# Performance work log

Hardware: AMD Instinct MI355X
Metric: run time of the kernel (lower is better)

## Reference

```python
import jax, jax.numpy as jnp
import numpy as np

H = 128          # hidden_channels
N_USER = 100000
N_ITEM = 50000
E = 1000000      # number of labeled edges


def setup_inputs() -> dict:
    key = jax.random.key(0)
    ks = jax.random.split(key, 6)
    z_user = jax.random.normal(ks[0], (N_USER, H), dtype=jnp.float32)
    z_item = jax.random.normal(ks[1], (N_ITEM, H), dtype=jnp.float32)
    row = jax.random.randint(ks[2], (E,), 0, N_USER, dtype=jnp.int64 if jax.config.jax_enable_x64 else jnp.int32)
    col = jax.random.randint(ks[3], (E,), 0, N_ITEM, dtype=jnp.int64 if jax.config.jax_enable_x64 else jnp.int32)
    W1 = jax.random.normal(ks[4], (2 * H, H), dtype=jnp.float32) / np.sqrt(2 * H)
    b1 = jnp.zeros((H,), dtype=jnp.float32)
    W2 = jax.random.normal(ks[5], (H, 1), dtype=jnp.float32) / np.sqrt(H)
    b2 = jnp.zeros((1,), dtype=jnp.float32)
    return {"z_user": z_user, "z_item": z_item, "row": row, "col": col,
            "W1": W1, "b1": b1, "W2": W2, "b2": b2}


def reference(z_user, z_item, row, col, W1, b1, W2, b2):
    # z = cat([z_user[row], z_item[col]], -1); lin1(z).relu(); lin2 -> view(-1)
    # Split W1 so we never materialize the [E, 2H] concat explicitly as one buffer:
    # cat([a, b]) @ W1 == a @ W1[:H] + b @ W1[H:]
    W1u, W1i = W1[:H], W1[H:]
    h = z_user[row] @ W1u + z_item[col] @ W1i + b1          # [E, H]
    h = jax.nn.relu(h)
    out = h @ W2 + b2                                        # [E, 1]
    return out.reshape(-1)
```

## Files before the change

kernel.cpp:

```cpp
#include <hip/hip_runtime.h>

#define HH 128
#define BU 8
#define BI 16
#define NBKT (BU * BI)
#define SCHUNK 2048
#define GPUC 8192

typedef __attribute__((ext_vector_type(8))) short bf16x8;
typedef __attribute__((ext_vector_type(4))) float f32x4;
typedef _Float16 h2 __attribute__((ext_vector_type(2)));

#if __has_builtin(__builtin_amdgcn_fdot2)
#define FDOT2(a, b, c) __builtin_amdgcn_fdot2((a), (b), (c), false)
#else
#define FDOT2(a, b, c) ((c) + (float)(a)[0] * (float)(b)[0] + (float)(a)[1] * (float)(b)[1])
#endif

__device__ inline unsigned short f2bf(float f) {
    unsigned u = __builtin_bit_cast(unsigned, f);
    u += 0x7FFF + ((u >> 16) & 1);
    return (unsigned short)(u >> 16);
}
__device__ inline unsigned short f2h(float f) {
    return __builtin_bit_cast(unsigned short, (_Float16)f);
}

__global__ __launch_bounds__(256) void wt_kernel(
    const float* __restrict__ W1, unsigned short* __restrict__ Wt)
{
    const int gid = blockIdx.x * 256 + threadIdx.x;
    const int h   = gid >> 11;
    const int c   = (gid >> 4) & 127;
    const int kc  = gid & 15;
    const float* src = W1 + (size_t)(h * 128 + kc * 8) * HH + c;
    unsigned short v[8];
    #pragma unroll
    for (int d = 0; d < 8; ++d)
        v[d] = f2bf(src[(size_t)d * HH]);
    uint4 pack;
    pack.x = (unsigned)v[0] | ((unsigned)v[1] << 16);
    pack.y = (unsigned)v[2] | ((unsigned)v[3] << 16);
    pack.z = (unsigned)v[4] | ((unsigned)v[5] << 16);
    pack.w = (unsigned)v[6] | ((unsigned)v[7] << 16);
    *(uint4*)(Wt + (size_t)h * 16384 + c * 128 + ((kc ^ (c & 15)) << 3)) = pack;
}

__global__ __launch_bounds__(256) void scatter_kernel(
    const int* __restrict__ row, const int* __restrict__ col,
    unsigned* __restrict__ cursor, unsigned* __restrict__ srt,
    unsigned* __restrict__ invpos, int E, unsigned n_user, unsigned n_item, int cap)
{
    __shared__ unsigned lh[NBKT];
    __shared__ unsigned gb[NBKT];
    __shared__ unsigned lc[NBKT];
    const int t    = threadIdx.x;
    const int base = blockIdx.x * SCHUNK;

    int uu[SCHUNK / 256], ii[SCHUNK / 256];
    if (t < NBKT) lh[t] = 0;
    __syncthreads();
    #pragma unroll
    for (int k = 0; k < SCHUNK / 256; ++k) {
        int e = base + k * 256 + t;
        if (e < E) {
            uu[k] = row[e]; ii[k] = col[e];
            unsigned uc = ((unsigned)uu[k] * BU) / n_user;
            unsigned ic = ((unsigned)ii[k] * BI) / n_item;
            atomicAdd(&lh[uc * BI + ic], 1u);
        }
    }
    __syncthreads();
    if (t < NBKT) {
        gb[t] = lh[t] ? (unsigned)(t * cap) + atomicAdd(&cursor[t], lh[t]) : 0u;
        lc[t] = 0;
    }
    __syncthreads();
    #pragma unroll
    for (int k = 0; k < SCHUNK / 256; ++k) {
        int e = base + k * 256 + t;
        if (e < E) {
            unsigned uc = ((unsigned)uu[k] * BU) / n_user;
            unsigned ic = ((unsigned)ii[k] * BI) / n_item;
            int b = (int)(uc * BI + ic);
            unsigned ucbase = (uc * n_user + 7u) >> 3;
            unsigned r   = atomicAdd(&lc[b], 1u);
            unsigned pos = gb[b] + r;
            srt[pos]  = (((unsigned)uu[k] - ucbase) << 16) | (unsigned)ii[k];
            invpos[e] = pos;
        }
    }
}

__global__ __launch_bounds__(256) void project_kernel(
    const float* __restrict__ Zu, const float* __restrict__ Zi,
    const unsigned short* __restrict__ Wt, const float* __restrict__ b1,
    unsigned short* __restrict__ Pu, unsigned short* __restrict__ Pi,
    int n_user, int n_item, int utiles, int itiles)
{
    __shared__ unsigned short sWt[128 * 128];
    __shared__ unsigned short sOut[64 * 136];

    const int t    = threadIdx.x;
    const int wave = t >> 6;
    const int lane = t & 63;
    const int l16  = lane & 15;
    const int lk8  = (lane >> 4) * 8;
    const int total = utiles + itiles;

    int staged = -1;

    for (int tid = blockIdx.x; tid < total; tid += gridDim.x) {
        const bool isUser = (tid < utiles);
        const int  half   = isUser ? 0 : 1;
        const float* __restrict__ Z = isUser ? Zu : Zi;
        unsigned short* __restrict__ P = isUser ? Pu : Pi;
        const int nrows = isUser ? n_user : n_item;
        const int rbase = (isUser ? tid : (tid - utiles)) << 6;

        if (half != staged) {
            __syncthreads();
            const unsigned short* src = Wt + (size_t)half * 16384;
            #pragma unroll
            for (int i = 0; i < 16; ++i) {
                int off = (i * 256 + t) * 8;
                *(uint4*)(sWt + off) = *(const uint4*)(src + off);
            }
            __syncthreads();
            staged = half;
        }

        float b1r[8];
        #pragma unroll
        for (int nt = 0; nt < 8; ++nt)
            b1r[nt] = isUser ? b1[nt * 16 + l16] : 0.f;

        f32x4 acc[8];
        #pragma unroll
        for (int nt = 0; nt < 8; ++nt) acc[nt] = (f32x4)0.f;

        int m = rbase + wave * 16 + l16;
        if (m > nrows - 1) m = nrows - 1;
        const float* Zrow = Z + (size_t)m * HH;

        #pragma unroll
        for (int kk = 0; kk < 4; ++kk) {
            float4 z0 = *(const float4*)(Zrow + kk * 32 + lk8);
            float4 z1 = *(const float4*)(Zrow + kk * 32 + lk8 + 4);
            bf16x8 a;
            a[0] = (short)f2bf(z0.x); a[1] = (short)f2bf(z0.y);
            a[2] = (short)f2bf(z0.z); a[3] = (short)f2bf(z0.w);
            a[4] = (short)f2bf(z1.x); a[5] = (short)f2bf(z1.y);
            a[6] = (short)f2bf(z1.z); a[7] = (short)f2bf(z1.w);

            const int chunkSw = ((kk * 4 + (lane >> 4)) ^ l16) << 3;
            #pragma unroll
            for (int nt = 0; nt < 8; ++nt) {
                int c = nt * 16 + l16;
                bf16x8 b = *(const bf16x8*)(sWt + c * 128 + chunkSw);
                acc[nt] = __builtin_amdgcn_mfma_f32_16x16x32_bf16(a, b, acc[nt], 0, 0, 0);
            }
        }

        __syncthreads();
        #pragma unroll
        for (int nt = 0; nt < 8; ++nt) {
            int colc = nt * 16 + l16;
            #pragma unroll
            for (int r = 0; r < 4; ++r) {
                int orow = wave * 16 + (lane >> 4) * 4 + r;
                sOut[orow * 136 + colc] = f2h(acc[nt][r] + b1r[nt]);
            }
        }
        __syncthreads();
        #pragma unroll
        for (int i = 0; i < 4; ++i) {
            int idx = t + i * 256;
            int r   = idx >> 4;
            int ch  = idx & 15;
            int grow = rbase + r;
            if (grow < nrows)
                *(uint4*)(P + (size_t)grow * HH + ch * 8) =
                    *(const uint4*)(sOut + r * 136 + ch * 8);
        }
    }
}

__global__ __launch_bounds__(256) void edge_sorted_kernel(
    const unsigned short* __restrict__ Pu, const unsigned short* __restrict__ Pi,
    const unsigned* __restrict__ srt, const unsigned* __restrict__ cursor,
    const float* __restrict__ W2, const float* __restrict__ b2,
    float* __restrict__ psorted, int cap, int n_user)
{
    const int uc     = blockIdx.x & (BU - 1);
    const int jj     = blockIdx.x >> 3;
    const int g      = threadIdx.x >> 3;
    const int lane8  = threadIdx.x & 7;
    const int gg     = jj * 32 + g;
    const int c0     = lane8 * 16;
    const int ucbase = (int)(((unsigned)uc * (unsigned)n_user + 7u) >> 3);

    h2 w2h[8];
    #pragma unroll
    for (int j = 0; j < 8; ++j) {
        w2h[j][0] = (_Float16)W2[c0 + 2 * j];
        w2h[j][1] = (_Float16)W2[c0 + 2 * j + 1];
    }
    const float b2s = b2[0];
    const h2 hz = {(_Float16)0, (_Float16)0};

    #pragma unroll 1
    for (int ic = 0; ic < BI; ++ic) {
        const int b    = uc * BI + ic;
        const int S    = b * cap;
        const int Tend = S + (int)cursor[b];
        for (int p = S + gg; p < Tend; p += GPUC) {
            unsigned pk = srt[p];
            int u  = ucbase + (int)(pk >> 16);
            int it = (int)(pk & 0xFFFFu);
            const unsigned short* pur = Pu + (size_t)u  * HH + c0;
            const unsigned short* pir = Pi + (size_t)it * HH + c0;
            uint4 a0 = *(const uint4*)pur;
            uint4 a1 = *(const uint4*)(pur + 8);
            uint4 c0v = *(const uint4*)pir;
            uint4 c1v = *(const uint4*)(pir + 8);
            unsigned aw[8] = {a0.x, a0.y, a0.z, a0.w, a1.x, a1.y, a1.z, a1.w};
            unsigned cw[8] = {c0v.x, c0v.y, c0v.z, c0v.w, c1v.x, c1v.y, c1v.z, c1v.w};
            float acc = 0.f;
            #pragma unroll
            for (int q = 0; q < 8; ++q) {
                h2 s = __builtin_bit_cast(h2, aw[q]) + __builtin_bit_cast(h2, cw[q]);
                s = __builtin_elementwise_max(s, hz);
                acc = FDOT2(s, w2h[q], acc);
            }
            acc += __shfl_xor(acc, 4, 64);
            acc += __shfl_xor(acc, 2, 64);
            acc += __shfl_xor(acc, 1, 64);
            if (lane8 == 0) psorted[p] = acc + b2s;
        }
    }
}

__global__ __launch_bounds__(256) void permute_kernel(
    const float* __restrict__ psorted, const unsigned* __restrict__ invpos,
    float* __restrict__ out, int E)
{
    int i  = blockIdx.x * blockDim.x + threadIdx.x;
    int st = gridDim.x * blockDim.x;
    for (int e = i; e < E; e += st)
        out[e] = psorted[invpos[e]];
}

__global__ __launch_bounds__(256) void edge_fp16_kernel(
    const unsigned short* __restrict__ Pu, const unsigned short* __restrict__ Pi,
    const int* __restrict__ row, const int* __restrict__ col,
    const float* __restrict__ W2, const float* __restrict__ b2,
    float* __restrict__ out, int E)
{
    const int lane8  = threadIdx.x & 7;
    const int gid    = (blockIdx.x * blockDim.x + threadIdx.x) >> 3;
    const int stride = (gridDim.x * blockDim.x) >> 3;
    const int c0     = lane8 * 16;

    h2 w2h[8];
    #pragma unroll
    for (int j = 0; j < 8; ++j) {
        w2h[j][0] = (_Float16)W2[c0 + 2 * j];
        w2h[j][1] = (_Float16)W2[c0 + 2 * j + 1];
    }
    const float b2s = b2[0];
    const h2 hz = {(_Float16)0, (_Float16)0};

    for (int e = gid; e < E; e += stride) {
        int u = row[e], it = col[e];
        const unsigned short* pur = Pu + (size_t)u  * HH + c0;
        const unsigned short* pir = Pi + (size_t)it * HH + c0;
        uint4 a0 = *(const uint4*)pur;
        uint4 a1 = *(const uint4*)(pur + 8);
        uint4 c0v = *(const uint4*)pir;
        uint4 c1v = *(const uint4*)(pir + 8);
        unsigned aw[8] = {a0.x, a0.y, a0.z, a0.w, a1.x, a1.y, a1.z, a1.w};
        unsigned cw[8] = {c0v.x, c0v.y, c0v.z, c0v.w, c1v.x, c1v.y, c1v.z, c1v.w};
        float acc = 0.f;
        #pragma unroll
        for (int q = 0; q < 8; ++q) {
            h2 s = __builtin_bit_cast(h2, aw[q]) + __builtin_bit_cast(h2, cw[q]);
            s = __builtin_elementwise_max(s, hz);
            acc = FDOT2(s, w2h[q], acc);
        }
        acc += __shfl_xor(acc, 4, 64);
        acc += __shfl_xor(acc, 2, 64);
        acc += __shfl_xor(acc, 1, 64);
        if (lane8 == 0) out[e] = acc + b2s;
    }
}

__global__ __launch_bounds__(256) void edge_direct_kernel(
    const float* __restrict__ zu, const float* __restrict__ zi,
    const int* __restrict__ row, const int* __restrict__ col,
    const float* __restrict__ W1, const float* __restrict__ b1,
    const float* __restrict__ W2, const float* __restrict__ b2,
    float* __restrict__ out, int E)
{
    const int lane   = threadIdx.x & 31;
    const int gid    = (blockIdx.x * blockDim.x + threadIdx.x) >> 5;
    const int stride = (gridDim.x * blockDim.x) >> 5;
    const int c0     = lane * 4;

    const float4 b1v = *(const float4*)(b1 + c0);
    const float4 w2v = *(const float4*)(W2 + c0);
    const float  b2s = b2[0];

    for (int e = gid; e < E; e += stride) {
        int u  = row[e];
        int it = col[e];
        const float* zur = zu + (size_t)u  * HH;
        const float* zir = zi + (size_t)it * HH;
        float4 acc = b1v;
        for (int k = 0; k < HH; ++k) {
            float  zk = zur[k];
            float4 w  = *(const float4*)(W1 + (size_t)k * HH + c0);
            acc.x = fmaf(zk, w.x, acc.x);
            acc.y = fmaf(zk, w.y, acc.y);
            acc.z = fmaf(zk, w.z, acc.z);
            acc.w = fmaf(zk, w.w, acc.w);
        }
        for (int k = 0; k < HH; ++k) {
            float  zk = zir[k];
            float4 w  = *(const float4*)(W1 + (size_t)(HH + k) * HH + c0);
            acc.x = fmaf(zk, w.x, acc.x);
            acc.y = fmaf(zk, w.y, acc.y);
            acc.z = fmaf(zk, w.z, acc.z);
            acc.w = fmaf(zk, w.w, acc.w);
        }
        float p = fmaxf(acc.x, 0.f) * w2v.x;
        p = fmaf(fmaxf(acc.y, 0.f), w2v.y, p);
        p = fmaf(fmaxf(acc.z, 0.f), w2v.z, p);
        p = fmaf(fmaxf(acc.w, 0.f), w2v.w, p);
        #pragma unroll
        for (int m = 16; m >= 1; m >>= 1)
            p += __shfl_xor(p, m, 64);
        if (lane == 0) out[e] = p + b2s;
    }
}

static inline size_t align256(size_t x) { return (x + 255) & ~(size_t)255; }

extern "C" void kernel_launch(void* const* d_in, const int* in_sizes, int n_in,
                              void* d_out, int out_size, void* d_ws, size_t ws_size,
                              hipStream_t stream)
{
    const float* z_user = (const float*)d_in[0];
    const float* z_item = (const float*)d_in[1];
    const int*   row    = (const int*)d_in[2];
    const int*   col    = (const int*)d_in[3];
    const float* W1     = (const float*)d_in[4];
    const float* b1     = (const float*)d_in[5];
    const float* W2     = (const float*)d_in[6];
    const float* b2     = (const float*)d_in[7];
    float*       out    = (float*)d_out;

    const int n_user = in_sizes[0] / HH;
    const int n_item = in_sizes[1] / HH;
    const int E      = in_sizes[2];

    const int capBase = (E + NBKT - 1) / NBKT;
    const int cap     = capBase + capBase / 4 + 64;
    const size_t padded = (size_t)cap * NBKT;

    const size_t offWt  = 0;
    const size_t offPu  = align256(offWt  + 32768 * 2);
    const size_t offPi  = align256(offPu  + (size_t)n_user * HH * 2);
    const size_t offSrt = align256(offPi  + (size_t)n_item * HH * 2);
    const size_t offPs  = align256(offSrt + padded * 4);
    const size_t offInv = align256(offPs  + padded * 4);
    const size_t offCur = align256(offInv + (size_t)E * 4);
    const size_t needSort = align256(offCur + NBKT * 4);
    const size_t needProj = align256(offPi + (size_t)n_item * HH * 2);

    const bool sortable = (n_user >= BU) && (n_item >= BI) &&
                          (n_item < 65536) && (n_user / BU + 1 < 65536) &&
                          (n_user <= (1 << 17)) && (ws_size >= needSort);

    const int utiles = (n_user + 63) >> 6;
    const int itiles = (n_item + 63) >> 6;
    const int total  = utiles + itiles;
    const int pgrid  = total < 768 ? total : 768;
    const int scatBlocks = (E + SCHUNK - 1) / SCHUNK;

    if (sortable) {
        unsigned short* Wt  = (unsigned short*)((char*)d_ws + offWt);
        unsigned short* Pu  = (unsigned short*)((char*)d_ws + offPu);
        unsigned short* Pi  = (unsigned short*)((char*)d_ws + offPi);
        unsigned*       srt = (unsigned*)((char*)d_ws + offSrt);
        float*          ps  = (float*)((char*)d_ws + offPs);
        unsigned*       inv = (unsigned*)((char*)d_ws + offInv);
        unsigned*       cur = (unsigned*)((char*)d_ws + offCur);

        hipMemsetAsync(cur, 0, NBKT * 4, stream);
        wt_kernel<<<16, 256, 0, stream>>>(W1, Wt);
        scatter_kernel<<<scatBlocks, 256, 0, stream>>>(
            row, col, cur, srt, inv, E, (unsigned)n_user, (unsigned)n_item, cap);
        project_kernel<<<pgrid, 256, 0, stream>>>(
            z_user, z_item, Wt, b1, Pu, Pi, n_user, n_item, utiles, itiles);
        edge_sorted_kernel<<<2048, 256, 0, stream>>>(Pu, Pi, srt, cur, W2, b2, ps, cap, n_user);
        permute_kernel<<<1024, 256, 0, stream>>>(ps, inv, out, E);
    } else if (ws_size >= needProj) {
        unsigned short* Wt = (unsigned short*)((char*)d_ws + offWt);
        unsigned short* Pu = (unsigned short*)((char*)d_ws + offPu);
        unsigned short* Pi = (unsigned short*)((char*)d_ws + offPi);
        wt_kernel<<<16, 256, 0, stream>>>(W1, Wt);
        project_kernel<<<pgrid, 256, 0, stream>>>(
            z_user, z_item, Wt, b1, Pu, Pi, n_user, n_item, utiles, itiles);
        edge_fp16_kernel<<<2048, 256, 0, stream>>>(Pu, Pi, row, col, W2, b2, out, E);
    } else {
        edge_direct_kernel<<<2048, 256, 0, stream>>>(z_user, z_item, row, col, W1, b1, W2, b2, out, E);
    }
}
```

Measured before the change: 100.8 us.

## Replace padded bucket capacity with histogram prefix-scan and read weights from global

Adds a histogram pass fused with the weight conversion, plus a single-block exclusive scan, so sorted edges are packed contiguously instead of into fixed-capacity padded buckets. Bucket count doubles along the item axis, and the edge kernel walks one contiguous range per user chunk rather than looping over padded sub-buckets. The projection kernel drops its shared-memory weight staging, reads the unswizzled weights directly from global/L2, and its grid grows to 2048 blocks. This trades an extra pass over row/col and an extra launch for less padding, better occupancy and fewer per-block weight loads.

```diff
diff --git a/kernel.cpp b/kernel.cpp
--- a/kernel.cpp
+++ b/kernel.cpp
@@ -2,7 +2,7 @@
 
 #define HH 128
 #define BU 8
-#define BI 16
+#define BI 32
 #define NBKT (BU * BI)
 #define SCHUNK 2048
 #define GPUC 8192
@@ -26,30 +26,71 @@
     return __builtin_bit_cast(unsigned short, (_Float16)f);
 }
 
-__global__ __launch_bounds__(256) void wt_kernel(
-    const float* __restrict__ W1, unsigned short* __restrict__ Wt)
-{
-    const int gid = blockIdx.x * 256 + threadIdx.x;
-    const int h   = gid >> 11;
-    const int c   = (gid >> 4) & 127;
-    const int kc  = gid & 15;
-    const float* src = W1 + (size_t)(h * 128 + kc * 8) * HH + c;
-    unsigned short v[8];
-    #pragma unroll
-    for (int d = 0; d < 8; ++d)
-        v[d] = f2bf(src[(size_t)d * HH]);
-    uint4 pack;
-    pack.x = (unsigned)v[0] | ((unsigned)v[1] << 16);
-    pack.y = (unsigned)v[2] | ((unsigned)v[3] << 16);
-    pack.z = (unsigned)v[4] | ((unsigned)v[5] << 16);
-    pack.w = (unsigned)v[6] | ((unsigned)v[7] << 16);
-    *(uint4*)(Wt + (size_t)h * 16384 + c * 128 + ((kc ^ (c & 15)) << 3)) = pack;
+__global__ __launch_bounds__(256) void prep_kernel(
+    const float* __restrict__ W1, unsigned short* __restrict__ Wt,
+    const int* __restrict__ row, const int* __restrict__ col,
+    unsigned* __restrict__ hist, int E, unsigned n_user, unsigned n_item)
+{
+    const int t = threadIdx.x;
+    if ((int)blockIdx.x < 16) {
+        const int gid = blockIdx.x * 256 + t;
+        const int h   = gid >> 11;
+        const int c   = (gid >> 4) & 127;
+        const int kc  = gid & 15;
+        const float* src = W1 + (size_t)(h * 128 + kc * 8) * HH + c;
+        unsigned short v[8];
+        #pragma unroll
+        for (int d = 0; d < 8; ++d)
+            v[d] = f2bf(src[(size_t)d * HH]);
+        uint4 pack;
+        pack.x = (unsigned)v[0] | ((unsigned)v[1] << 16);
+        pack.y = (unsigned)v[2] | ((unsigned)v[3] << 16);
+        pack.z = (unsigned)v[4] | ((unsigned)v[5] << 16);
+        pack.w = (unsigned)v[6] | ((unsigned)v[7] << 16);
+        *(uint4*)(Wt + (size_t)h * 16384 + c * 128 + kc * 8) = pack;
+        return;
+    }
+    __shared__ unsigned lh[NBKT];
+    lh[t] = 0;
+    __syncthreads();
+    const int base = ((int)blockIdx.x - 16) * SCHUNK;
+    #pragma unroll
+    for (int k = 0; k < SCHUNK / 256; ++k) {
+        int e = base + k * 256 + t;
+        if (e < E) {
+            unsigned uc = ((unsigned)row[e] * BU) / n_user;
+            unsigned ic = ((unsigned)col[e] * BI) / n_item;
+            atomicAdd(&lh[uc * BI + ic], 1u);
+        }
+    }
+    __syncthreads();
+    if (lh[t]) atomicAdd(&hist[t], lh[t]);
+}
+
+__global__ __launch_bounds__(256) void scan256_kernel(
+    const unsigned* __restrict__ hist, unsigned* __restrict__ cursor,
+    unsigned* __restrict__ bstart)
+{
+    __shared__ unsigned s[NBKT];
+    const int t = threadIdx.x;
+    unsigned v = hist[t];
+    s[t] = v; __syncthreads();
+    for (int off = 1; off < NBKT; off <<= 1) {
+        unsigned x = (t >= off) ? s[t - off] : 0u;
+        __syncthreads();
+        s[t] += x;
+        __syncthreads();
+    }
+    unsigned excl = s[t] - v;
+    cursor[t] = excl;
+    bstart[t] = excl;
+    if (t == NBKT - 1) bstart[NBKT] = s[t];
 }
 
 __global__ __launch_bounds__(256) void scatter_kernel(
     const int* __restrict__ row, const int* __restrict__ col,
     unsigned* __restrict__ cursor, unsigned* __restrict__ srt,
-    unsigned* __restrict__ invpos, int E, unsigned n_user, unsigned n_item, int cap)
+    unsigned* __restrict__ invpos, int E, unsigned n_user, unsigned n_item)
 {
     __shared__ unsigned lh[NBKT];
     __shared__ unsigned gb[NBKT];
@@ -58,7 +99,7 @@
     const int base = blockIdx.x * SCHUNK;
 
     int uu[SCHUNK / 256], ii[SCHUNK / 256];
-    if (t < NBKT) lh[t] = 0;
+    lh[t] = 0;
     __syncthreads();
     #pragma unroll
     for (int k = 0; k < SCHUNK / 256; ++k) {
@@ -71,10 +112,8 @@
         }
     }
     __syncthreads();
-    if (t < NBKT) {
-        gb[t] = lh[t] ? (unsigned)(t * cap) + atomicAdd(&cursor[t], lh[t]) : 0u;
-        lc[t] = 0;
-    }
+    gb[t] = lh[t] ? atomicAdd(&cursor[t], lh[t]) : 0u;
+    lc[t] = 0;
     __syncthreads();
     #pragma unroll
     for (int k = 0; k < SCHUNK / 256; ++k) {
@@ -98,7 +137,6 @@
     unsigned short* __restrict__ Pu, unsigned short* __restrict__ Pi,
     int n_user, int n_item, int utiles, int itiles)
 {
-    __shared__ unsigned short sWt[128 * 128];
     __shared__ unsigned short sOut[64 * 136];
 
     const int t    = threadIdx.x;
@@ -108,32 +146,18 @@
     const int lk8  = (lane >> 4) * 8;
     const int total = utiles + itiles;
 
-    int staged = -1;
+    float b1r[8];
+    #pragma unroll
+    for (int nt = 0; nt < 8; ++nt)
+        b1r[nt] = b1[nt * 16 + l16];
 
     for (int tid = blockIdx.x; tid < total; tid += gridDim.x) {
         const bool isUser = (tid < utiles);
-        const int  half   = isUser ? 0 : 1;
         const float* __restrict__ Z = isUser ? Zu : Zi;
         unsigned short* __restrict__ P = isUser ? Pu : Pi;
+        const unsigned short* __restrict__ Wh = Wt + (isUser ? 0 : 16384);
         const int nrows = isUser ? n_user : n_item;
         const int rbase = (isUser ? tid : (tid - utiles)) << 6;
-
-        if (half != staged) {
-            __syncthreads();
-            const unsigned short* src = Wt + (size_t)half * 16384;
-            #pragma unroll
-            for (int i = 0; i < 16; ++i) {
-                int off = (i * 256 + t) * 8;
-                *(uint4*)(sWt + off) = *(const uint4*)(src + off);
-            }
-            __syncthreads();
-            staged = half;
-        }
-
-        float b1r[8];
-        #pragma unroll
-        for (int nt = 0; nt < 8; ++nt)
-            b1r[nt] = isUser ? b1[nt * 16 + l16] : 0.f;
 
         f32x4 acc[8];
         #pragma unroll
@@ -153,11 +177,11 @@
             a[4] = (short)f2bf(z1.x); a[5] = (short)f2bf(z1.y);
             a[6] = (short)f2bf(z1.z); a[7] = (short)f2bf(z1.w);
 
-            const int chunkSw = ((kk * 4 + (lane >> 4)) ^ l16) << 3;
+            const int chunk = (kk * 4 + (lane >> 4)) * 8;
             #pragma unroll
             for (int nt = 0; nt < 8; ++nt) {
                 int c = nt * 16 + l16;
-                bf16x8 b = *(const bf16x8*)(sWt + c * 128 + chunkSw);
+                bf16x8 b = *(const bf16x8*)(Wh + c * 128 + chunk);
                 acc[nt] = __builtin_amdgcn_mfma_f32_16x16x32_bf16(a, b, acc[nt], 0, 0, 0);
             }
         }
@@ -166,10 +190,11 @@
         #pragma unroll
         for (int nt = 0; nt < 8; ++nt) {
             int colc = nt * 16 + l16;
+            float bias = isUser ? b1r[nt] : 0.f;
             #pragma unroll
             for (int r = 0; r < 4; ++r) {
                 int orow = wave * 16 + (lane >> 4) * 4 + r;
-                sOut[orow * 136 + colc] = f2h(acc[nt][r] + b1r[nt]);
+                sOut[orow * 136 + colc] = f2h(acc[nt][r] + bias);
             }
         }
         __syncthreads();
@@ -188,9 +213,9 @@
 
 __global__ __launch_bounds__(256) void edge_sorted_kernel(
     const unsigned short* __restrict__ Pu, const unsigned short* __restrict__ Pi,
-    const unsigned* __restrict__ srt, const unsigned* __restrict__ cursor,
+    const unsigned* __restrict__ srt, const unsigned* __restrict__ bstart,
     const float* __restrict__ W2, const float* __restrict__ b2,
-    float* __restrict__ psorted, int cap, int n_user)
+    float* __restrict__ psorted, int n_user)
 {
     const int uc     = blockIdx.x & (BU - 1);
     const int jj     = blockIdx.x >> 3;
@@ -200,6 +225,9 @@
     const int c0     = lane8 * 16;
     const int ucbase = (int)(((unsigned)uc * (unsigned)n_user + 7u) >> 3);
 
+    const int S = (int)bstart[uc * BI];
+    const int T = (int)bstart[(uc + 1) * BI];
+
     h2 w2h[8];
     #pragma unroll
     for (int j = 0; j < 8; ++j) {
@@ -209,35 +237,30 @@
     const float b2s = b2[0];
     const h2 hz = {(_Float16)0, (_Float16)0};
 
-    #pragma unroll 1
-    for (int ic = 0; ic < BI; ++ic) {
-        const int b    = uc * BI + ic;
-        const int S    = b * cap;
-        const int Tend = S + (int)cursor[b];
-        for (int p = S + gg; p < Tend; p += GPUC) {
-            unsigned pk = srt[p];
-            int u  = ucbase + (int)(pk >> 16);
-            int it = (int)(pk & 0xFFFFu);
-            const unsigned short* pur = Pu + (size_t)u  * HH + c0;
-            const unsigned short* pir = Pi + (size_t)it * HH + c0;
-            uint4 a0 = *(const uint4*)pur;
-            uint4 a1 = *(const uint4*)(pur + 8);
-            uint4 c0v = *(const uint4*)pir;
-            uint4 c1v = *(const uint4*)(pir + 8);
-            unsigned aw[8] = {a0.x, a0.y, a0.z, a0.w, a1.x, a1.y, a1.z, a1.w};
-            unsigned cw[8] = {c0v.x, c0v.y, c0v.z, c0v.w, c1v.x, c1v.y, c1v.z, c1v.w};
-            float acc = 0.f;
-            #pragma unroll
-            for (int q = 0; q < 8; ++q) {
-                h2 s = __builtin_bit_cast(h2, aw[q]) + __builtin_bit_cast(h2, cw[q]);
-                s = __builtin_elementwise_max(s, hz);
-                acc = FDOT2(s, w2h[q], acc);
-            }
-            acc += __shfl_xor(acc, 4, 64);
-            acc += __shfl_xor(acc, 2, 64);
-            acc += __shfl_xor(acc, 1, 64);
-            if (lane8 == 0) psorted[p] = acc + b2s;
-        }
+    #pragma unroll 2
+    for (int p = S + gg; p < T; p += GPUC) {
+        unsigned pk = srt[p];
+        int u  = ucbase + (int)(pk >> 16);
+        int it = (int)(pk & 0xFFFFu);
+        const unsigned short* pur = Pu + (size_t)u  * HH + c0;
+        const unsigned short* pir = Pi + (size_t)it * HH + c0;
+        uint4 a0 = *(const uint4*)pur;
+        uint4 a1 = *(const uint4*)(pur + 8);
+        uint4 c0v = *(const uint4*)pir;
+        uint4 c1v = *(const uint4*)(pir + 8);
+        unsigned aw[8] = {a0.x, a0.y, a0.z, a0.w, a1.x, a1.y, a1.z, a1.w};
+        unsigned cw[8] = {c0v.x, c0v.y, c0v.z, c0v.w, c1v.x, c1v.y, c1v.z, c1v.w};
+        float acc = 0.f;
+        #pragma unroll
+        for (int q = 0; q < 8; ++q) {
+            h2 s = __builtin_bit_cast(h2, aw[q]) + __builtin_bit_cast(h2, cw[q]);
+            s = __builtin_elementwise_max(s, hz);
+            acc = FDOT2(s, w2h[q], acc);
+        }
+        acc += __shfl_xor(acc, 4, 64);
+        acc += __shfl_xor(acc, 2, 64);
+        acc += __shfl_xor(acc, 1, 64);
+        if (lane8 == 0) psorted[p] = acc + b2s;
     }
 }
 
@@ -364,18 +387,16 @@
     const int n_item = in_sizes[1] / HH;
     const int E      = in_sizes[2];
 
-    const int capBase = (E + NBKT - 1) / NBKT;
-    const int cap     = capBase + capBase / 4 + 64;
-    const size_t padded = (size_t)cap * NBKT;
-
     const size_t offWt  = 0;
     const size_t offPu  = align256(offWt  + 32768 * 2);
     const size_t offPi  = align256(offPu  + (size_t)n_user * HH * 2);
     const size_t offSrt = align256(offPi  + (size_t)n_item * HH * 2);
-    const size_t offPs  = align256(offSrt + padded * 4);
-    const size_t offInv = align256(offPs  + padded * 4);
+    const size_t offPs  = align256(offSrt + (size_t)E * 4);
+    const size_t offInv = align256(offPs  + (size_t)E * 4);
     const size_t offCur = align256(offInv + (size_t)E * 4);
-    const size_t needSort = align256(offCur + NBKT * 4);
+    const size_t offBst = align256(offCur + NBKT * 4);
+    const size_t offHist= align256(offBst + (NBKT + 1) * 4);
+    const size_t needSort = align256(offHist + NBKT * 4);
     const size_t needProj = align256(offPi + (size_t)n_item * HH * 2);
 
     const bool sortable = (n_user >= BU) && (n_item >= BI) &&
@@ -385,8 +406,8 @@
     const int utiles = (n_user + 63) >> 6;
     const int itiles = (n_item + 63) >> 6;
     const int total  = utiles + itiles;
-    const int pgrid  = total < 768 ? total : 768;
-    const int scatBlocks = (E + SCHUNK - 1) / SCHUNK;
+    const int pgrid  = total < 2048 ? total : 2048;
+    const int histBlocks = (E + SCHUNK - 1) / SCHUNK;
 
     if (sortable) {
         unsigned short* Wt  = (unsigned short*)((char*)d_ws + offWt);
@@ -396,20 +417,25 @@
         float*          ps  = (float*)((char*)d_ws + offPs);
         unsigned*       inv = (unsigned*)((char*)d_ws + offInv);
         unsigned*       cur = (unsigned*)((char*)d_ws + offCur);
-
-        hipMemsetAsync(cur, 0, NBKT * 4, stream);
-        wt_kernel<<<16, 256, 0, stream>>>(W1, Wt);
-        scatter_kernel<<<scatBlocks, 256, 0, stream>>>(
-            row, col, cur, srt, inv, E, (unsigned)n_user, (unsigned)n_item, cap);
+        unsigned*       bst = (unsigned*)((char*)d_ws + offBst);
+        unsigned*       hst = (unsigned*)((char*)d_ws + offHist);
+
+        hipMemsetAsync(hst, 0, NBKT * 4, stream);
+        prep_kernel<<<16 + histBlocks, 256, 0, stream>>>(
+            W1, Wt, row, col, hst, E, (unsigned)n_user, (unsigned)n_item);
+        scan256_kernel<<<1, NBKT, 0, stream>>>(hst, cur, bst);
+        scatter_kernel<<<histBlocks, 256, 0, stream>>>(
+            row, col, cur, srt, inv, E, (unsigned)n_user, (unsigned)n_item);
         project_kernel<<<pgrid, 256, 0, stream>>>(
             z_user, z_item, Wt, b1, Pu, Pi, n_user, n_item, utiles, itiles);
-        edge_sorted_kernel<<<2048, 256, 0, stream>>>(Pu, Pi, srt, cur, W2, b2, ps, cap, n_user);
+        edge_sorted_kernel<<<2048, 256, 0, stream>>>(Pu, Pi, srt, bst, W2, b2, ps, n_user);
         permute_kernel<<<1024, 256, 0, stream>>>(ps, inv, out, E);
     } else if (ws_size >= needProj) {
         unsigned short* Wt = (unsigned short*)((char*)d_ws + offWt);
         unsigned short* Pu = (unsigned short*)((char*)d_ws + offPu);
         unsigned short* Pi = (unsigned short*)((char*)d_ws + offPi);
-        wt_kernel<<<16, 256, 0, stream>>>(W1, Wt);
+        prep_kernel<<<16, 256, 0, stream>>>(
+            W1, Wt, row, col, (unsigned*)nullptr, 0, (unsigned)n_user, (unsigned)n_item);
         project_kernel<<<pgrid, 256, 0, stream>>>(
             z_user, z_item, Wt, b1, Pu, Pi, n_user, n_item, utiles, itiles);
         edge_fp16_kernel<<<2048, 256, 0, stream>>>(Pu, Pi, row, col, W2, b2, out, E);
```

New measurement: 142.7 us. 1.42x slower.
